# Performance work log

Hardware: AMD Instinct MI355X
Metric: run time of the kernel (lower is better)

## Reference

```python
import jax, jax.numpy as jnp
import numpy as np

B_BOXES = 5
N_CLASSES = 80
LAMBDA_COORD = 5.0
LAMBDA_NOOBJ = 0.5
LAMBDA_CLASS = 1.0
EPS = 1e-6


def _corners(b):
    # b: (..., 4) center-format (x, y, w, h) -> x1, y1, x2, y2
    x, y, w, h = b[..., 0], b[..., 1], b[..., 2], b[..., 3]
    return x - w / 2, y - h / 2, x + w / 2, y + h / 2


def pairwise_iou(p_box, t_box):
    # p_box, t_box: (N, S, S, B, 4) -> ious: (N, S, S, B_pred, B_tgt)
    px1, py1, px2, py2 = _corners(p_box[..., :, None, :])
    tx1, ty1, tx2, ty2 = _corners(t_box[..., None, :, :])
    iw = jnp.clip(jnp.minimum(px2, tx2) - jnp.maximum(px1, tx1), 0.0)
    ih = jnp.clip(jnp.minimum(py2, ty2) - jnp.maximum(py1, ty1), 0.0)
    inter = iw * ih
    area_p = (px2 - px1) * (py2 - py1)
    area_t = (tx2 - tx1) * (ty2 - ty1)
    return inter / (area_p + area_t - inter + EPS)


def setup_inputs() -> dict:
    key = jax.random.key(0)
    k1, k2 = jax.random.split(key)
    N, S = 128, 26
    ch = B_BOXES * (5 + N_CLASSES)  # 425
    preds = jax.random.normal(k1, (N, S, S, ch), dtype=jnp.float32)
    targets = jax.random.normal(k2, (N, S, S, ch), dtype=jnp.float32)
    return {"preds": preds, "targets": targets}


def reference(preds, targets):
    N, S = preds.shape[0], preds.shape[1]
    D = 5 + N_CLASSES
    p = preds.reshape(N, S, S, B_BOXES, D)
    t = targets.reshape(N, S, S, B_BOXES, D)

    ious = pairwise_iou(p[..., :4], t[..., :4])          # (N,S,S,B,B)
    best = jnp.argmax(ious, axis=-1)                      # (N,S,S,B)
    idx = jnp.broadcast_to(best[..., None], t.shape)
    matched = jnp.take_along_axis(t, idx, axis=3)         # (N,S,S,B,D)

    obj = (matched[..., 4] > 0).astype(p.dtype)           # (N,S,S,B)
    noobj = 1.0 - obj

    xy_loss = LAMBDA_COORD * jnp.sum(obj[..., None] * (p[..., 0:2] - matched[..., 0:2]) ** 2)

    pwh = jnp.sqrt(jnp.abs(p[..., 2:4] + EPS))
    twh = jnp.sqrt(jnp.abs(matched[..., 2:4] + EPS))
    wh_loss = LAMBDA_COORD * jnp.sum(obj[..., None] * (pwh - twh) ** 2)

    conf_sq = (p[..., 4] - matched[..., 4]) ** 2
    conf_loss_obj = jnp.sum(obj * conf_sq)
    conf_loss_noobj = LAMBDA_NOOBJ * jnp.sum(noobj * conf_sq)

    tcls = jnp.argmax(t[..., 5:], axis=-1)                # (N,S,S,B)
    logp = jax.nn.log_softmax(p[..., 5:], axis=-1)
    nll = -jnp.take_along_axis(logp, tcls[..., None], axis=-1)[..., 0]
    class_loss = LAMBDA_CLASS * jnp.sum(obj * nll)

    return xy_loss + wh_loss + conf_loss_obj + conf_loss_noobj + class_loss
```

## Files before the change

kernel.cpp:

```cpp
#include <hip/hip_runtime.h>
#include <math.h>

#define NB 5
#define NC 80
#define DD 85
#define CH 425
#define EPSF 1e-6f
#define CPB 8
#define TASKS (CPB * NB)
#define CHUNK_F (CPB * CH)
#define CHUNK_F4 (CHUNK_F / 4)
#define TPB 256
#define NK ((CHUNK_F4 + TPB - 1) / TPB)

__device__ __forceinline__ void gload_lds16(const float* g, float* l) {
    __builtin_amdgcn_global_load_lds(
        (const __attribute__((address_space(1))) void*)g,
        (__attribute__((address_space(3))) void*)l,
        16, 0, 0);
}

__global__ __launch_bounds__(TPB) void yolo_loss_kernel(
    const float* __restrict__ preds,
    const float* __restrict__ targets,
    float* __restrict__ partials,
    int use_atomic)
{
    __shared__ __align__(16) float s_p[CHUNK_F];
    __shared__ __align__(16) float s_t[CHUNK_F];
    __shared__ float s_wsum[4];

    const int tid  = threadIdx.x;
    const int wave = tid >> 6;
    const int lane = tid & 63;

    const float* gp = preds   + (size_t)blockIdx.x * CHUNK_F;
    const float* gt = targets + (size_t)blockIdx.x * CHUNK_F;

    #pragma unroll
    for (int k = 0; k < NK; ++k) {
        const int base = k * TPB + wave * 64;
        const int idx  = base + lane;
        if (idx < CHUNK_F4) {
            gload_lds16(gp + 4 * (size_t)idx, s_p + 4 * base);
            gload_lds16(gt + 4 * (size_t)idx, s_t + 4 * base);
        }
    }
    asm volatile("s_waitcnt vmcnt(0)" ::: "memory");
    __syncthreads();

    float acc = 0.0f;
    if (tid < 4 * TASKS) {
        const int t = tid >> 2;
        const int q = tid & 3;
        const int kb = t * DD + 5 + q * 20;

        float s  = 0.0f;
        float bv = -INFINITY;
        int   bi = 0x7fffffff;
        float bp = 0.0f;
        #pragma unroll 5
        for (int k = 0; k < 20; ++k) {
            const float pl = s_p[kb + k];
            const float tl = s_t[kb + k];
            s += __expf(pl);
            if (tl > bv) { bv = tl; bi = q * 20 + k; bp = pl; }
        }
        #pragma unroll
        for (int m = 1; m < 4; m <<= 1) {
            s += __shfl_xor(s, m, 64);
            const float ov = __shfl_xor(bv, m, 64);
            const int   oi = __shfl_xor(bi, m, 64);
            const float op = __shfl_xor(bp, m, 64);
            if (ov > bv || (ov == bv && oi < bi)) { bv = ov; bi = oi; bp = op; }
        }

        if (q == 0) {
            const float nll = __logf(s) - bp;

            const int c  = t / 5;
            const int pb = t * DD;
            const float px = s_p[pb + 0], py = s_p[pb + 1], pw = s_p[pb + 2],
                        ph = s_p[pb + 3], pconf = s_p[pb + 4];
            const float px1 = px - pw * 0.5f, py1 = py - ph * 0.5f;
            const float px2 = px + pw * 0.5f, py2 = py + ph * 0.5f;
            const float area_p = (px2 - px1) * (py2 - py1);

            float best = -INFINITY;
            float mx = 0.f, my = 0.f, mw = 0.f, mh = 0.f, mconf = 0.f;
            #pragma unroll
            for (int j = 0; j < NB; ++j) {
                const int tb = (c * NB + j) * DD;
                const float tx = s_t[tb + 0], ty = s_t[tb + 1], tw = s_t[tb + 2],
                            th = s_t[tb + 3], tcf = s_t[tb + 4];
                const float tx1 = tx - tw * 0.5f, ty1 = ty - th * 0.5f;
                const float tx2 = tx + tw * 0.5f, ty2 = ty + th * 0.5f;
                float iw = fminf(px2, tx2) - fmaxf(px1, tx1); iw = fmaxf(iw, 0.0f);
                float ih = fminf(py2, ty2) - fmaxf(py1, ty1); ih = fmaxf(ih, 0.0f);
                const float inter  = iw * ih;
                const float area_t = (tx2 - tx1) * (ty2 - ty1);
                const float iou    = inter / (area_p + area_t - inter + EPSF);
                if (iou > best) { best = iou; mx = tx; my = ty; mw = tw; mh = th; mconf = tcf; }
            }

            const float obj = (mconf > 0.0f) ? 1.0f : 0.0f;
            const float dx = px - mx, dy = py - my;
            float term = 5.0f * obj * (dx * dx + dy * dy);
            const float dw = sqrtf(fabsf(pw + EPSF)) - sqrtf(fabsf(mw + EPSF));
            const float dh = sqrtf(fabsf(ph + EPSF)) - sqrtf(fabsf(mh + EPSF));
            term += 5.0f * obj * (dw * dw + dh * dh);
            const float dc  = pconf - mconf;
            const float csq = dc * dc;
            term += obj * csq + 0.5f * (1.0f - obj) * csq;
            term += obj * nll;
            acc = term;
        }
    }

    #pragma unroll
    for (int off = 32; off > 0; off >>= 1) acc += __shfl_down(acc, off, 64);
    if ((tid & 63) == 0) s_wsum[tid >> 6] = acc;
    __syncthreads();
    if (tid == 0) {
        const float v = s_wsum[0] + s_wsum[1] + s_wsum[2] + s_wsum[3];
        if (use_atomic) atomicAdd(partials, v);
        else            partials[blockIdx.x] = v;
    }
}

__global__ __launch_bounds__(TPB) void reduce_kernel(
    const float* __restrict__ partials, float* __restrict__ out, int n)
{
    float s = 0.0f;
    for (int i = threadIdx.x; i < n; i += TPB) s += partials[i];
    #pragma unroll
    for (int off = 32; off > 0; off >>= 1) s += __shfl_down(s, off, 64);
    __shared__ float wsum[4];
    if ((threadIdx.x & 63) == 0) wsum[threadIdx.x >> 6] = s;
    __syncthreads();
    if (threadIdx.x == 0) out[0] = wsum[0] + wsum[1] + wsum[2] + wsum[3];
}

extern "C" void kernel_launch(void* const* d_in, const int* in_sizes, int n_in,
                              void* d_out, int out_size, void* d_ws, size_t ws_size,
                              hipStream_t stream) {
    const float* preds   = (const float*)d_in[0];
    const float* targets = (const float*)d_in[1];
    float* out = (float*)d_out;

    const int ncells = in_sizes[0] / CH;
    const int blocks = ncells / CPB;

    if (ws_size >= (size_t)blocks * sizeof(float)) {
        float* ws = (float*)d_ws;
        yolo_loss_kernel<<<blocks, TPB, 0, stream>>>(preds, targets, ws, 0);
        reduce_kernel<<<1, TPB, 0, stream>>>(ws, out, blocks);
    } else {
        hipMemsetAsync(out, 0, sizeof(float), stream);
        yolo_loss_kernel<<<blocks, TPB, 0, stream>>>(preds, targets, out, 1);
    }
}
```

Measured before the change: 308.1 us.

## Use persistent grid-stride blocks with double-buffered LDS async staging

Replaces the one-chunk-per-block launch with a grid capped at a fixed block count. Each block loops over 4-cell chunks and prefetches the next chunk into a second LDS buffer via global_load_lds while computing the current one. The goal is to overlap memory loads with compute and to cut block launch and tail overhead. In exchange it adds barriers per iteration and uses smaller chunks, so only 80 of 256 threads do work per chunk. It also clamps out-of-range lanes to redundant loads rather than skipping them.

```diff
diff --git a/kernel.cpp b/kernel.cpp
--- a/kernel.cpp
+++ b/kernel.cpp
@@ -6,12 +6,15 @@
 #define DD 85
 #define CH 425
 #define EPSF 1e-6f
-#define CPB 8
+
+#define CPB 4
 #define TASKS (CPB * NB)
 #define CHUNK_F (CPB * CH)
 #define CHUNK_F4 (CHUNK_F / 4)
 #define TPB 256
-#define NK ((CHUNK_F4 + TPB - 1) / TPB)
+#define ROUNDS 2
+#define SLOT_F4 (ROUNDS * TPB)
+#define MAXBLK 1280
 
 __device__ __forceinline__ void gload_lds16(const float* g, float* l) {
     __builtin_amdgcn_global_load_lds(
@@ -20,109 +23,134 @@
         16, 0, 0);
 }
 
+__device__ __forceinline__ void stage_chunk(const float* __restrict__ preds,
+                                            const float* __restrict__ targets,
+                                            int chunk, float* lp, float* lt,
+                                            int wave, int lane) {
+    const float* gp = preds   + (size_t)chunk * CHUNK_F;
+    const float* gt = targets + (size_t)chunk * CHUNK_F;
+    #pragma unroll
+    for (int r = 0; r < ROUNDS; ++r) {
+        const int base = r * TPB + wave * 64;
+        int idx = base + lane;
+        if (idx > CHUNK_F4 - 1) idx = CHUNK_F4 - 1;
+        gload_lds16(gp + 4 * (size_t)idx, lp + 4 * base);
+        gload_lds16(gt + 4 * (size_t)idx, lt + 4 * base);
+    }
+}
+
 __global__ __launch_bounds__(TPB) void yolo_loss_kernel(
     const float* __restrict__ preds,
     const float* __restrict__ targets,
     float* __restrict__ partials,
+    int nchunks,
     int use_atomic)
 {
-    __shared__ __align__(16) float s_p[CHUNK_F];
-    __shared__ __align__(16) float s_t[CHUNK_F];
-    __shared__ float s_wsum[4];
+    __shared__ __align__(16) float s_p[2][SLOT_F4 * 4];
+    __shared__ __align__(16) float s_t[2][SLOT_F4 * 4];
 
     const int tid  = threadIdx.x;
     const int wave = tid >> 6;
     const int lane = tid & 63;
-
-    const float* gp = preds   + (size_t)blockIdx.x * CHUNK_F;
-    const float* gt = targets + (size_t)blockIdx.x * CHUNK_F;
-
-    #pragma unroll
-    for (int k = 0; k < NK; ++k) {
-        const int base = k * TPB + wave * 64;
-        const int idx  = base + lane;
-        if (idx < CHUNK_F4) {
-            gload_lds16(gp + 4 * (size_t)idx, s_p + 4 * base);
-            gload_lds16(gt + 4 * (size_t)idx, s_t + 4 * base);
-        }
-    }
-    asm volatile("s_waitcnt vmcnt(0)" ::: "memory");
-    __syncthreads();
+    const int stride = gridDim.x;
 
     float acc = 0.0f;
-    if (tid < 4 * TASKS) {
-        const int t = tid >> 2;
-        const int q = tid & 3;
-        const int kb = t * DD + 5 + q * 20;
+    int   cur = 0;
+    int   c   = blockIdx.x;
 
-        float s  = 0.0f;
-        float bv = -INFINITY;
-        int   bi = 0x7fffffff;
-        float bp = 0.0f;
-        #pragma unroll 5
-        for (int k = 0; k < 20; ++k) {
-            const float pl = s_p[kb + k];
-            const float tl = s_t[kb + k];
-            s += __expf(pl);
-            if (tl > bv) { bv = tl; bi = q * 20 + k; bp = pl; }
+    if (c < nchunks)
+        stage_chunk(preds, targets, c, s_p[0], s_t[0], wave, lane);
+
+    for (; c < nchunks; c += stride) {
+        const int cn = c + stride;
+        if (cn < nchunks) {
+            stage_chunk(preds, targets, cn, s_p[cur ^ 1], s_t[cur ^ 1], wave, lane);
+            asm volatile("s_waitcnt vmcnt(4)" ::: "memory");
+        } else {
+            asm volatile("s_waitcnt vmcnt(0)" ::: "memory");
         }
-        #pragma unroll
-        for (int m = 1; m < 4; m <<= 1) {
-            s += __shfl_xor(s, m, 64);
-            const float ov = __shfl_xor(bv, m, 64);
-            const int   oi = __shfl_xor(bi, m, 64);
-            const float op = __shfl_xor(bp, m, 64);
-            if (ov > bv || (ov == bv && oi < bi)) { bv = ov; bi = oi; bp = op; }
+        asm volatile("s_barrier" ::: "memory");
+
+        const float* sp = s_p[cur];
+        const float* st = s_t[cur];
+
+        if (tid < 4 * TASKS) {
+            const int t = tid >> 2;
+            const int q = tid & 3;
+            const int kb = t * DD + 5 + q * 20;
+
+            float s  = 0.0f;
+            float bv = -INFINITY;
+            int   bi = 0x7fffffff;
+            float bp = 0.0f;
+            #pragma unroll 5
+            for (int k = 0; k < 20; ++k) {
+                const float pl = sp[kb + k];
+                const float tl = st[kb + k];
+                s += __expf(pl);
+                if (tl > bv) { bv = tl; bi = q * 20 + k; bp = pl; }
+            }
+            #pragma unroll
+            for (int m = 1; m < 4; m <<= 1) {
+                s += __shfl_xor(s, m, 64);
+                const float ov = __shfl_xor(bv, m, 64);
+                const int   oi = __shfl_xor(bi, m, 64);
+                const float op = __shfl_xor(bp, m, 64);
+                if (ov > bv || (ov == bv && oi < bi)) { bv = ov; bi = oi; bp = op; }
+            }
+
+            if (q == 0) {
+                const float nll = __logf(s) - bp;
+
+                const int cell = t / 5;
+                const int pb   = t * DD;
+                const float px = sp[pb + 0], py = sp[pb + 1], pw = sp[pb + 2],
+                            ph = sp[pb + 3], pconf = sp[pb + 4];
+                const float px1 = px - pw * 0.5f, py1 = py - ph * 0.5f;
+                const float px2 = px + pw * 0.5f, py2 = py + ph * 0.5f;
+                const float area_p = (px2 - px1) * (py2 - py1);
+
+                float best = -INFINITY;
+                float mx = 0.f, my = 0.f, mw = 0.f, mh = 0.f, mconf = 0.f;
+                #pragma unroll
+                for (int j = 0; j < NB; ++j) {
+                    const int tb = (cell * NB + j) * DD;
+                    const float tx = st[tb + 0], ty = st[tb + 1], tw = st[tb + 2],
+                                th = st[tb + 3], tcf = st[tb + 4];
+                    const float tx1 = tx - tw * 0.5f, ty1 = ty - th * 0.5f;
+                    const float tx2 = tx + tw * 0.5f, ty2 = ty + th * 0.5f;
+                    float iw = fminf(px2, tx2) - fmaxf(px1, tx1); iw = fmaxf(iw, 0.0f);
+                    float ih = fminf(py2, ty2) - fmaxf(py1, ty1); ih = fmaxf(ih, 0.0f);
+                    const float inter  = iw * ih;
+                    const float area_t = (tx2 - tx1) * (ty2 - ty1);
+                    const float iou    = inter / (area_p + area_t - inter + EPSF);
+                    if (iou > best) { best = iou; mx = tx; my = ty; mw = tw; mh = th; mconf = tcf; }
+                }
+
+                const float obj = (mconf > 0.0f) ? 1.0f : 0.0f;
+                const float dx = px - mx, dy = py - my;
+                float term = 5.0f * obj * (dx * dx + dy * dy);
+                const float dw = sqrtf(fabsf(pw + EPSF)) - sqrtf(fabsf(mw + EPSF));
+                const float dh = sqrtf(fabsf(ph + EPSF)) - sqrtf(fabsf(mh + EPSF));
+                term += 5.0f * obj * (dw * dw + dh * dh);
+                const float dc  = pconf - mconf;
+                const float csq = dc * dc;
+                term += obj * csq + 0.5f * (1.0f - obj) * csq;
+                term += obj * nll;
+                acc += term;
+            }
         }
 
-        if (q == 0) {
-            const float nll = __logf(s) - bp;
-
-            const int c  = t / 5;
-            const int pb = t * DD;
-            const float px = s_p[pb + 0], py = s_p[pb + 1], pw = s_p[pb + 2],
-                        ph = s_p[pb + 3], pconf = s_p[pb + 4];
-            const float px1 = px - pw * 0.5f, py1 = py - ph * 0.5f;
-            const float px2 = px + pw * 0.5f, py2 = py + ph * 0.5f;
-            const float area_p = (px2 - px1) * (py2 - py1);
-
-            float best = -INFINITY;
-            float mx = 0.f, my = 0.f, mw = 0.f, mh = 0.f, mconf = 0.f;
-            #pragma unroll
-            for (int j = 0; j < NB; ++j) {
-                const int tb = (c * NB + j) * DD;
-                const float tx = s_t[tb + 0], ty = s_t[tb + 1], tw = s_t[tb + 2],
-                            th = s_t[tb + 3], tcf = s_t[tb + 4];
-                const float tx1 = tx - tw * 0.5f, ty1 = ty - th * 0.5f;
-                const float tx2 = tx + tw * 0.5f, ty2 = ty + th * 0.5f;
-                float iw = fminf(px2, tx2) - fmaxf(px1, tx1); iw = fmaxf(iw, 0.0f);
-                float ih = fminf(py2, ty2) - fmaxf(py1, ty1); ih = fmaxf(ih, 0.0f);
-                const float inter  = iw * ih;
-                const float area_t = (tx2 - tx1) * (ty2 - ty1);
-                const float iou    = inter / (area_p + area_t - inter + EPSF);
-                if (iou > best) { best = iou; mx = tx; my = ty; mw = tw; mh = th; mconf = tcf; }
-            }
-
-            const float obj = (mconf > 0.0f) ? 1.0f : 0.0f;
-            const float dx = px - mx, dy = py - my;
-            float term = 5.0f * obj * (dx * dx + dy * dy);
-            const float dw = sqrtf(fabsf(pw + EPSF)) - sqrtf(fabsf(mw + EPSF));
-            const float dh = sqrtf(fabsf(ph + EPSF)) - sqrtf(fabsf(mh + EPSF));
-            term += 5.0f * obj * (dw * dw + dh * dh);
-            const float dc  = pconf - mconf;
-            const float csq = dc * dc;
-            term += obj * csq + 0.5f * (1.0f - obj) * csq;
-            term += obj * nll;
-            acc = term;
-        }
+        asm volatile("s_barrier" ::: "memory");
+        cur ^= 1;
     }
 
     #pragma unroll
     for (int off = 32; off > 0; off >>= 1) acc += __shfl_down(acc, off, 64);
-    if ((tid & 63) == 0) s_wsum[tid >> 6] = acc;
+    if (lane == 0) s_p[0][wave] = acc;
     __syncthreads();
     if (tid == 0) {
-        const float v = s_wsum[0] + s_wsum[1] + s_wsum[2] + s_wsum[3];
+        const float v = s_p[0][0] + s_p[0][1] + s_p[0][2] + s_p[0][3];
         if (use_atomic) atomicAdd(partials, v);
         else            partials[blockIdx.x] = v;
     }
@@ -148,15 +176,16 @@
     const float* targets = (const float*)d_in[1];
     float* out = (float*)d_out;
 
-    const int ncells = in_sizes[0] / CH;
-    const int blocks = ncells / CPB;
+    const int ncells  = in_sizes[0] / CH;
+    const int nchunks = ncells / CPB;
+    const int blocks  = nchunks < MAXBLK ? nchunks : MAXBLK;
 
     if (ws_size >= (size_t)blocks * sizeof(float)) {
         float* ws = (float*)d_ws;
-        yolo_loss_kernel<<<blocks, TPB, 0, stream>>>(preds, targets, ws, 0);
+        yolo_loss_kernel<<<blocks, TPB, 0, stream>>>(preds, targets, ws, nchunks, 0);
         reduce_kernel<<<1, TPB, 0, stream>>>(ws, out, blocks);
     } else {
         hipMemsetAsync(out, 0, sizeof(float), stream);
-        yolo_loss_kernel<<<blocks, TPB, 0, stream>>>(preds, targets, out, 1);
+        yolo_loss_kernel<<<blocks, TPB, 0, stream>>>(preds, targets, out, nchunks, 1);
     }
 }
```

Measured after the change: 329.7 us. 7.0% more time.

## Replace LDS staging with direct global loads in a grid-stride box loop

Applied to the files above, without the earlier changes.

Removes the global-to-LDS async staging of 8-cell chunks and instead has each quad of threads read its box's class logits and box fields directly from global memory. It uses a fixed grid of 2048 blocks with a grid-stride loop over boxes, which keeps every thread busy, unlike the old layout where only 160 of 256 threads computed. The cost is strided, uncoalesced 4-byte global loads (each thread reads 20 consecutive floats, and neighbouring quads are 340 bytes apart) in place of wide 16-byte coalesced copies, so it relies on caches to merge accesses.

```diff
diff --git a/kernel.cpp b/kernel.cpp
--- a/kernel.cpp
+++ b/kernel.cpp
@@ -6,63 +6,35 @@
 #define DD 85
 #define CH 425
 #define EPSF 1e-6f
-#define CPB 8
-#define TASKS (CPB * NB)
-#define CHUNK_F (CPB * CH)
-#define CHUNK_F4 (CHUNK_F / 4)
 #define TPB 256
-#define NK ((CHUNK_F4 + TPB - 1) / TPB)
-
-__device__ __forceinline__ void gload_lds16(const float* g, float* l) {
-    __builtin_amdgcn_global_load_lds(
-        (const __attribute__((address_space(1))) void*)g,
-        (__attribute__((address_space(3))) void*)l,
-        16, 0, 0);
-}
+#define GRID 2048
 
 __global__ __launch_bounds__(TPB) void yolo_loss_kernel(
     const float* __restrict__ preds,
     const float* __restrict__ targets,
     float* __restrict__ partials,
+    int nboxes,
     int use_atomic)
 {
-    __shared__ __align__(16) float s_p[CHUNK_F];
-    __shared__ __align__(16) float s_t[CHUNK_F];
-    __shared__ float s_wsum[4];
-
-    const int tid  = threadIdx.x;
-    const int wave = tid >> 6;
-    const int lane = tid & 63;
-
-    const float* gp = preds   + (size_t)blockIdx.x * CHUNK_F;
-    const float* gt = targets + (size_t)blockIdx.x * CHUNK_F;
-
-    #pragma unroll
-    for (int k = 0; k < NK; ++k) {
-        const int base = k * TPB + wave * 64;
-        const int idx  = base + lane;
-        if (idx < CHUNK_F4) {
-            gload_lds16(gp + 4 * (size_t)idx, s_p + 4 * base);
-            gload_lds16(gt + 4 * (size_t)idx, s_t + 4 * base);
-        }
-    }
-    asm volatile("s_waitcnt vmcnt(0)" ::: "memory");
-    __syncthreads();
+    const int tid     = threadIdx.x;
+    const int q       = tid & 3;
+    const int quad0   = (blockIdx.x * TPB + tid) >> 2;
+    const int qstride = (gridDim.x * TPB) >> 2;
 
     float acc = 0.0f;
-    if (tid < 4 * TASKS) {
-        const int t = tid >> 2;
-        const int q = tid & 3;
-        const int kb = t * DD + 5 + q * 20;
+
+    for (int g = quad0; g < nboxes; g += qstride) {
+        const int base = g * DD;
+        const int kb   = base + 5 + q * 20;
 
         float s  = 0.0f;
         float bv = -INFINITY;
         int   bi = 0x7fffffff;
         float bp = 0.0f;
-        #pragma unroll 5
+        #pragma unroll
         for (int k = 0; k < 20; ++k) {
-            const float pl = s_p[kb + k];
-            const float tl = s_t[kb + k];
+            const float pl = preds[kb + k];
+            const float tl = targets[kb + k];
             s += __expf(pl);
             if (tl > bv) { bv = tl; bi = q * 20 + k; bp = pl; }
         }
@@ -78,10 +50,10 @@
         if (q == 0) {
             const float nll = __logf(s) - bp;
 
-            const int c  = t / 5;
-            const int pb = t * DD;
-            const float px = s_p[pb + 0], py = s_p[pb + 1], pw = s_p[pb + 2],
-                        ph = s_p[pb + 3], pconf = s_p[pb + 4];
+            const int cell = g / 5;
+            const float px = preds[base + 0], py = preds[base + 1],
+                        pw = preds[base + 2], ph = preds[base + 3],
+                        pconf = preds[base + 4];
             const float px1 = px - pw * 0.5f, py1 = py - ph * 0.5f;
             const float px2 = px + pw * 0.5f, py2 = py + ph * 0.5f;
             const float area_p = (px2 - px1) * (py2 - py1);
@@ -90,9 +62,10 @@
             float mx = 0.f, my = 0.f, mw = 0.f, mh = 0.f, mconf = 0.f;
             #pragma unroll
             for (int j = 0; j < NB; ++j) {
-                const int tb = (c * NB + j) * DD;
-                const float tx = s_t[tb + 0], ty = s_t[tb + 1], tw = s_t[tb + 2],
-                            th = s_t[tb + 3], tcf = s_t[tb + 4];
+                const int tb = (cell * NB + j) * DD;
+                const float tx = targets[tb + 0], ty = targets[tb + 1],
+                            tw = targets[tb + 2], th = targets[tb + 3],
+                            tcf = targets[tb + 4];
                 const float tx1 = tx - tw * 0.5f, ty1 = ty - th * 0.5f;
                 const float tx2 = tx + tw * 0.5f, ty2 = ty + th * 0.5f;
                 float iw = fminf(px2, tx2) - fmaxf(px1, tx1); iw = fmaxf(iw, 0.0f);
@@ -113,10 +86,11 @@
             const float csq = dc * dc;
             term += obj * csq + 0.5f * (1.0f - obj) * csq;
             term += obj * nll;
-            acc = term;
+            acc += term;
         }
     }
 
+    __shared__ float s_wsum[4];
     #pragma unroll
     for (int off = 32; off > 0; off >>= 1) acc += __shfl_down(acc, off, 64);
     if ((tid & 63) == 0) s_wsum[tid >> 6] = acc;
@@ -149,14 +123,15 @@
     float* out = (float*)d_out;
 
     const int ncells = in_sizes[0] / CH;
-    const int blocks = ncells / CPB;
+    const int nboxes = ncells * NB;
+    const int blocks = GRID;
 
     if (ws_size >= (size_t)blocks * sizeof(float)) {
         float* ws = (float*)d_ws;
-        yolo_loss_kernel<<<blocks, TPB, 0, stream>>>(preds, targets, ws, 0);
+        yolo_loss_kernel<<<blocks, TPB, 0, stream>>>(preds, targets, ws, nboxes, 0);
         reduce_kernel<<<1, TPB, 0, stream>>>(ws, out, blocks);
     } else {
         hipMemsetAsync(out, 0, sizeof(float), stream);
-        yolo_loss_kernel<<<blocks, TPB, 0, stream>>>(preds, targets, out, 1);
+        yolo_loss_kernel<<<blocks, TPB, 0, stream>>>(preds, targets, out, nboxes, 1);
     }
 }
```

Result: no change. 313.0 us (+1.6%).
